# Optimization experiments

Measured on AMD Instinct MI355X. Metric: run time of the kernel, lower is better.

## Reference

```python
import jax, jax.numpy as jnp
import numpy as np

# config derived from init_kwargs: batch_sizes=[2048,2048], rs=[32,128], num_adapters=[32,32]
B1, B2, MULT = 2048, 2048, 4            # group1 tokens (r_mult=1), group2 tokens (r_mult=128/32=4)
IN_F, OUT_F, R_MIN = 4096, 4096, 32
NA1, NA2 = 32, 32
N_SPLIT_ADAPTERS = NA1 + NA2 * MULT      # 160 rank-min slices
LORA_BATCH = B1 + B2 * MULT              # 10240 gathered rows


def setup_inputs() -> dict:
    key = jax.random.key(0)
    k1, k2, k3, k4, k5 = jax.random.split(key, 5)
    x = jax.random.normal(k1, (B1 + B2, 1, IN_F), dtype=jnp.float16)
    lora_A = (jax.random.normal(k2, (N_SPLIT_ADAPTERS, IN_F, R_MIN), dtype=jnp.float16) * jnp.float16(0.02))
    lora_B = (jax.random.normal(k3, (N_SPLIT_ADAPTERS, R_MIN, OUT_F), dtype=jnp.float16) * jnp.float16(0.02))
    # group1: one row per token; group2: each token repeated MULT times (rank split)
    xids = jnp.concatenate([
        jnp.arange(B1, dtype=jnp.int32),
        jnp.repeat(jnp.arange(B1, B1 + B2, dtype=jnp.int32), MULT),
    ])
    # group1 adapters occupy slice ids [0, NA1); group2 adapter j occupies NA1 + j*MULT .. +MULT-1
    w1 = jax.random.randint(k4, (B1,), 0, NA1, dtype=jnp.int32)
    j = jax.random.randint(k5, (B2,), 0, NA2, dtype=jnp.int32)
    w2 = ((jnp.int32(NA1) + j * MULT)[:, None] + jnp.arange(MULT, dtype=jnp.int32)[None, :]).reshape(-1)
    wids = jnp.concatenate([w1, w2])
    return {"x": x, "xids": xids, "wids": wids, "lora_A": lora_A, "lora_B": lora_B}


def reference(x, xids, wids, lora_A, lora_B):
    xg = jnp.take(x, xids, axis=0)          # (L, 1, IN_F)
    A = jnp.take(lora_A, wids, axis=0)      # (L, IN_F, R_MIN)
    Bw = jnp.take(lora_B, wids, axis=0)     # (L, R_MIN, OUT_F)
    y = jnp.einsum('lpi,lir->lpr', xg, A)   # (L, 1, R_MIN)
    y = jnp.einsum('lpr,lro->lpo', y, Bw) * 2.0  # (L, 1, OUT_F), scaling factor 2.0
    # split + sum combine: group1 passes through, group2 sums each block of MULT rank-slices
    z1 = y[:B1]                                          # (B1, 1, OUT_F)
    z2 = y[B1:].reshape(B2, MULT, 1, OUT_F).sum(axis=1)  # (B2, 1, OUT_F)
    return jnp.concatenate([z1, z2], axis=0)             # (B1+B2, 1, OUT_F)
```

## Files before the change

### kernel.cpp

```cpp
#include <hip/hip_runtime.h>

#define IN_F   4096
#define OUT_F  4096
#define RK     32
#define NB1    2048
#define MAXB   2048
#define LBATCH 10240
#define LRK    (LBATCH * RK)

typedef __attribute__((ext_vector_type(2))) __fp16 h2;
typedef __attribute__((ext_vector_type(4))) __fp16 h4;
typedef __attribute__((ext_vector_type(8))) __fp16 h8;
typedef __attribute__((ext_vector_type(4))) float  f4;


__global__ __launch_bounds__(256) void bin_rows(const int* __restrict__ wids,
                                                int* __restrict__ cnt,
                                                int* __restrict__ list) {
    __shared__ int lc;
    int g = blockIdx.x, t = threadIdx.x;
    if (t == 0) lc = 0;
    __syncthreads();
    int* lg = list + g * MAXB;
    if (g < 32) {
        for (int i = t; i < NB1; i += 256)
            if (wids[i] == g) lg[atomicAdd(&lc, 1)] = i;
    } else {
        for (int i = t; i < 2048; i += 256)
            if (32 + ((wids[NB1 + 4 * i] - 32) >> 2) == g) lg[atomicAdd(&lc, 1)] = i;
    }
    __syncthreads();
    if (t == 0) cnt[g] = lc;
}

__device__ __forceinline__ void lda(const float* __restrict__ As, int s,
                                    int kp0, int c40, f4 L[2][2]) {
    #pragma unroll
    for (int p = 0; p < 2; ++p) {
        const float* q = As + ((size_t)s * 32 + 2 * (kp0 + 8 * p)) * RK + c40;
        L[p][0] = *(const f4*)q;
        L[p][1] = *(const f4*)(q + RK);
    }
}
__device__ __forceinline__ void wra(__fp16 (*dst)[40], int kp0, int c40,
                                    const f4 L[2][2]) {
    #pragma unroll
    for (int p = 0; p < 2; ++p) {
        int k = 2 * (kp0 + 8 * p);
        #pragma unroll
        for (int j = 0; j < 4; ++j) {
            int c  = c40 + j;
            int kb = (k >> 3) ^ ((c >> 3) & 3);
            *(h2*)&dst[c][kb * 8 + (k & 7)] =
                __builtin_amdgcn_cvt_pkrtz(L[p][0][j], L[p][1][j]);
        }
    }
}

template<int NST, int PITCH>
__device__ __forceinline__ void s1_waveloop(const float* __restrict__ Ap,
                                            const __fp16 (*Xl)[PITCH],
                                            __fp16 (*buf)[32][40], int koff0,
                                            int m, int kg, int kp0, int c40,
                                            f4& acc0, f4& acc1) {
    f4 L0[2][2], L1[2][2];
    lda(Ap, 0, kp0, c40, L0);
    wra(buf[0], kp0, c40, L0);
    if (NST > 1) lda(Ap, 1, kp0, c40, L1);
    #pragma unroll
    for (int s = 0; s < NST; ++s) {
        h8 xa = *(const h8*)&Xl[m][koff0 + s * 32 + kg * 8];
        int c0 = m,      kb0 = kg ^ ((c0 >> 3) & 3);
        int c1 = m + 16, kb1 = kg ^ ((c1 >> 3) & 3);
        h8 bf0 = *(const h8*)&buf[s & 1][c0][kb0 * 8];
        h8 bf1 = *(const h8*)&buf[s & 1][c1][kb1 * 8];
        if (s + 2 < NST) lda(Ap, s + 2, kp0, c40, ((s & 1) == 0) ? L0 : L1);
        acc0 = __builtin_amdgcn_mfma_f32_16x16x32_f16(xa, bf0, acc0, 0, 0, 0);
        acc1 = __builtin_amdgcn_mfma_f32_16x16x32_f16(xa, bf1, acc1, 0, 0, 0);
        if (s + 1 < NST) wra(buf[(s + 1) & 1], kp0, c40, ((s & 1) == 0) ? L1 : L0);
    }
}

template<int KS>
__global__ __launch_bounds__(256, 4) void s1(const float* __restrict__ x,
                                             const float* __restrict__ A,
                                             const int* __restrict__ cnt,
                                             const int* __restrict__ list,
                                             float* __restrict__ slabs) {
    constexpr int KCH   = IN_F / KS;
    constexpr int PITCH = KCH + 8;
    constexpr int C4    = KCH / 4;
    __shared__ __fp16 Xl[16][PITCH];
    __shared__ __fp16 At[4][2][32][40];
    __shared__ int rowid[16];

    int t = threadIdx.x, lane = t & 63, wv = t >> 6;
    int m = lane & 15, kg = lane >> 4;
    int bx = blockIdx.x, kc = blockIdx.y, rt = blockIdx.z;
    int p2 = bx >= 32;
    int n = cnt[bx];
    if (rt * 16 >= n) return;
    const int* lst = list + bx * MAXB;
    if (t < 16) {
        int it = rt * 16 + t;
        rowid[t] = lst[it < n ? it : n - 1];
    }
    __syncthreads();

    {
        int k0 = kc * KCH;
        #pragma unroll
        for (int itr = 0; itr < KCH / 64; ++itr) {
            int slot = t + 256 * itr;
            int row  = slot / C4;
            int c4   = slot & (C4 - 1);
            int xrow = rowid[row] + (p2 ? NB1 : 0);
            f4 v = *(const f4*)&x[(size_t)xrow * IN_F + k0 + 4 * c4];
            h4 pk;
            h2 a = __builtin_amdgcn_cvt_pkrtz(v.x, v.y);
            h2 b = __builtin_amdgcn_cvt_pkrtz(v.z, v.w);
            pk[0] = a.x; pk[1] = a.y; pk[2] = b.x; pk[3] = b.y;
            *(h4*)&Xl[row][4 * c4] = pk;
        }
    }
    __syncthreads();

    int kp0 = lane >> 3, c40 = (lane & 7) * 4;
    f4 acc0 = {0.f, 0.f, 0.f, 0.f}, acc1 = {0.f, 0.f, 0.f, 0.f};
    float* slab = slabs + (size_t)kc * LRK;

    if (p2) {
        int u = bx - 32;
        const float* Ap = A + ((size_t)(32 + 4 * u + wv) * IN_F + (size_t)kc * KCH) * RK;
        s1_waveloop<KCH / 32, PITCH>(Ap, Xl, At[wv], 0, m, kg, kp0, c40, acc0, acc1);
        #pragma unroll
        for (int q = 0; q < 4; ++q) {
            int itq = rt * 16 + 4 * kg + q;
            if (itq < n) {
                int rid = rowid[4 * kg + q];
                float* sp = slab + (size_t)(NB1 + 4 * rid + wv) * RK + m;
                sp[0]  = acc0[q];
                sp[16] = acc1[q];
            }
        }
    } else {
        const float* Ap = A + ((size_t)bx * IN_F + (size_t)kc * KCH + wv * (KCH / 4)) * RK;
        s1_waveloop<KCH / 128, PITCH>(Ap, Xl, At[wv], wv * (KCH / 4), m, kg, kp0, c40, acc0, acc1);
        float* red = (float*)&Xl[0][0];
        __syncthreads();
        if (wv > 0) {
            *(f4*)&red[((wv - 1) * 64 + lane) * 8]     = acc0;
            *(f4*)&red[((wv - 1) * 64 + lane) * 8 + 4] = acc1;
        }
        __syncthreads();
        if (wv == 0) {
            #pragma unroll
            for (int j = 0; j < 3; ++j) {
                acc0 += *(const f4*)&red[(j * 64 + lane) * 8];
                acc1 += *(const f4*)&red[(j * 64 + lane) * 8 + 4];
            }
            #pragma unroll
            for (int q = 0; q < 4; ++q) {
                int itq = rt * 16 + 4 * kg + q;
                if (itq < n) {
                    int rid = rowid[4 * kg + q];
                    float* sp = slab + (size_t)rid * RK + m;
                    sp[0]  = acc0[q];
                    sp[16] = acc1[q];
                }
            }
        }
    }
}

template<int KS>
__global__ __launch_bounds__(256) void reduceR(const float* __restrict__ slabs,
                                               __fp16* __restrict__ Rh) {
    int i = (blockIdx.x * 256 + threadIdx.x) * 8;
    f4 a = *(const f4*)(slabs + i);
    f4 b = *(const f4*)(slabs + i + 4);
    #pragma unroll
    for (int s = 1; s < KS; ++s) {
        a += *(const f4*)(slabs + (size_t)s * LRK + i);
        b += *(const f4*)(slabs + (size_t)s * LRK + i + 4);
    }
    h8 o;
    o[0] = (__fp16)a.x; o[1] = (__fp16)a.y; o[2] = (__fp16)a.z; o[3] = (__fp16)a.w;
    o[4] = (__fp16)b.x; o[5] = (__fp16)b.y; o[6] = (__fp16)b.z; o[7] = (__fp16)b.w;
    *(h8*)(Rh + i) = o;
}

__global__ __launch_bounds__(256, 4) void s2(const __fp16* __restrict__ Rh,
                                             const float* __restrict__ B,
                                             const int* __restrict__ cnt,
                                             const int* __restrict__ list,
                                             float* __restrict__ out) {
    int lane = threadIdx.x & 63, wv = threadIdx.x >> 6;
    int g   = blockIdx.x;
    int oct = blockIdx.y * 4 + wv;
    int p2  = g >= 32;
    int n = cnt[g];
    if (n == 0) return;
    const int* lst = list + g * MAXB;
    int m = lane & 15, kg = lane >> 4;
    int oc0 = oct * 32;
    int nkc = p2 ? 4 : 1;

    h8 bf[4][2];
    #pragma unroll
    for (int kcb = 0; kcb < 4; ++kcb) {
        if (kcb < nkc) {
            int a = p2 ? (32 + 4 * (g - 32) + kcb) : g;
            const float* Bb = B + ((size_t)a * RK + kg * 8) * OUT_F + oc0 + m;
            #pragma unroll
            for (int ct = 0; ct < 2; ++ct) {
                union { h8 v; h2 h[4]; } u2;
                #pragma unroll
                for (int jj = 0; jj < 4; ++jj) {
                    float e0 = Bb[(size_t)(2 * jj) * OUT_F + ct * 16];
                    float e1 = Bb[(size_t)(2 * jj + 1) * OUT_F + ct * 16];
                    u2.h[jj] = __builtin_amdgcn_cvt_pkrtz(e0, e1);
                }
                bf[kcb][ct] = u2.v;
            }
        }
    }

    for (int rt = 0; rt * 16 < n; ++rt) {
        int it = rt * 16 + m;
        int ridm = lst[it < n ? it : n - 1];
        f4 acc0 = {0.f, 0.f, 0.f, 0.f}, acc1 = {0.f, 0.f, 0.f, 0.f};
        #pragma unroll
        for (int kcb = 0; kcb < 4; ++kcb) {
            if (kcb < nkc) {
                int rrow = p2 ? (NB1 + 4 * ridm + kcb) : ridm;
                h8 rf = *(const h8*)(Rh + (size_t)rrow * RK + kg * 8);
                acc0 = __builtin_amdgcn_mfma_f32_16x16x32_f16(rf, bf[kcb][0], acc0, 0, 0, 0);
                acc1 = __builtin_amdgcn_mfma_f32_16x16x32_f16(rf, bf[kcb][1], acc1, 0, 0, 0);
            }
        }
        #pragma unroll
        for (int q = 0; q < 4; ++q) {
            int itq = rt * 16 + 4 * kg + q;
            if (itq < n) {
                int ridq = lst[itq];
                int orow = p2 ? (NB1 + ridq) : ridq;
                float* op = out + (size_t)orow * OUT_F + oc0 + m;
                op[0]  = 2.f * acc0[q];
                op[16] = 2.f * acc1[q];
            }
        }
    }
}

extern "C" void kernel_launch(void* const* d_in, const int* in_sizes, int n_in,
                              void* d_out, int out_size, void* d_ws, size_t ws_size,
                              hipStream_t stream) {
    const float* x    = (const float*)d_in[0];
    const int*   wids = (const int*)  d_in[2];
    const float* A    = (const float*)d_in[3];
    const float* Bm   = (const float*)d_in[4];
    float* out = (float*)d_out;

    int* wsI  = (int*)d_ws;
    int* cnt  = wsI;
    int* list = wsI + 64;
    __fp16* Rh  = (__fp16*)(list + 64 * MAXB);
    float* slabs = (float*)((char*)Rh + (size_t)LRK * sizeof(__fp16));

    size_t fixed = (size_t)(64 + 64 * MAXB) * sizeof(int) + (size_t)LRK * sizeof(__fp16);
    int ks = (ws_size >= fixed + (size_t)8 * LRK * sizeof(float)) ? 8 : 4;

    bin_rows<<<dim3(64), dim3(256), 0, stream>>>(wids, cnt, list);
    if (ks == 8) {
        s1<8><<<dim3(64, 8, 8), dim3(256), 0, stream>>>(x, A, cnt, list, slabs);
        reduceR<8><<<dim3(160), dim3(256), 0, stream>>>(slabs, Rh);
    } else {
        s1<4><<<dim3(64, 4, 8), dim3(256), 0, stream>>>(x, A, cnt, list, slabs);
        reduceR<4><<<dim3(160), dim3(256), 0, stream>>>(slabs, Rh);
    }
    s2<<<dim3(64, 32), dim3(256), 0, stream>>>(Rh, Bm, cnt, list, out);
}
```

Measured before the change: 305.8 us.

## Pre-transpose LoRA A to fp16 k-major and stream operands directly from global

Adds a prep pass, merged with the row-binning kernel, that converts lora_A from fp32 to fp16 and transposes it so each rank column is contiguous along K. The first-stage kernel then drops its LDS staging of x and A. Each lane loads its MFMA fragments straight from global memory: 8-element fp16 vectors for A, and x converted in registers. The aim is to halve A traffic in the main GEMV and remove LDS round trips and barriers. In exchange the whole A tensor is rewritten on every call, workspace use grows, and the stride-4096 fragment loads may coalesce poorly.

After: 325.0 us. 6.3% more time.

```diff
diff --git a/kernel.cpp b/kernel.cpp
--- a/kernel.cpp
+++ b/kernel.cpp
@@ -7,164 +7,151 @@
 #define MAXB   2048
 #define LBATCH 10240
 #define LRK    (LBATCH * RK)
+#define NADP   160
 
 typedef __attribute__((ext_vector_type(2))) __fp16 h2;
-typedef __attribute__((ext_vector_type(4))) __fp16 h4;
 typedef __attribute__((ext_vector_type(8))) __fp16 h8;
 typedef __attribute__((ext_vector_type(4))) float  f4;
 
 
-__global__ __launch_bounds__(256) void bin_rows(const int* __restrict__ wids,
-                                                int* __restrict__ cnt,
-                                                int* __restrict__ list) {
-    __shared__ int lc;
-    int g = blockIdx.x, t = threadIdx.x;
-    if (t == 0) lc = 0;
+__global__ __launch_bounds__(256) void prep(const int* __restrict__ wids,
+                                            int* __restrict__ cnt,
+                                            int* __restrict__ list,
+                                            const float* __restrict__ A,
+                                            __fp16* __restrict__ Ath) {
+    int bx = blockIdx.x, t = threadIdx.x;
+    if (bx < 64) {
+        __shared__ int lc;
+        if (t == 0) lc = 0;
+        __syncthreads();
+        int* lg = list + bx * MAXB;
+        if (bx < 32) {
+            for (int i = t; i < NB1; i += 256)
+                if (wids[i] == bx) lg[atomicAdd(&lc, 1)] = i;
+        } else {
+            for (int i = t; i < 2048; i += 256)
+                if (32 + ((wids[NB1 + 4 * i] - 32) >> 2) == bx) lg[atomicAdd(&lc, 1)] = i;
+        }
+        __syncthreads();
+        if (t == 0) cnt[bx] = lc;
+        return;
+    }
+    int bb = bx - 64;
+    int a = bb >> 4, kt = bb & 15, k0 = kt * 256;
+    __shared__ __fp16 T[32][264];
+    const float* Ab = A + ((size_t)a * IN_F + k0) * RK;
+    #pragma unroll
+    for (int i = 0; i < 8; ++i) {
+        int slot = t + 256 * i;
+        int k = slot >> 3, c4 = (slot & 7) * 4;
+        f4 v = *(const f4*)(Ab + (size_t)k * RK + c4);
+        T[c4 + 0][k] = (__fp16)v.x; T[c4 + 1][k] = (__fp16)v.y;
+        T[c4 + 2][k] = (__fp16)v.z; T[c4 + 3][k] = (__fp16)v.w;
+    }
     __syncthreads();
-    int* lg = list + g * MAXB;
-    if (g < 32) {
-        for (int i = t; i < NB1; i += 256)
-            if (wids[i] == g) lg[atomicAdd(&lc, 1)] = i;
-    } else {
-        for (int i = t; i < 2048; i += 256)
-            if (32 + ((wids[NB1 + 4 * i] - 32) >> 2) == g) lg[atomicAdd(&lc, 1)] = i;
-    }
-    __syncthreads();
-    if (t == 0) cnt[g] = lc;
-}
-
-__device__ __forceinline__ void lda(const float* __restrict__ As, int s,
-                                    int kp0, int c40, f4 L[2][2]) {
-    #pragma unroll
-    for (int p = 0; p < 2; ++p) {
-        const float* q = As + ((size_t)s * 32 + 2 * (kp0 + 8 * p)) * RK + c40;
-        L[p][0] = *(const f4*)q;
-        L[p][1] = *(const f4*)(q + RK);
-    }
-}
-__device__ __forceinline__ void wra(__fp16 (*dst)[40], int kp0, int c40,
-                                    const f4 L[2][2]) {
-    #pragma unroll
-    for (int p = 0; p < 2; ++p) {
-        int k = 2 * (kp0 + 8 * p);
-        #pragma unroll
-        for (int j = 0; j < 4; ++j) {
-            int c  = c40 + j;
-            int kb = (k >> 3) ^ ((c >> 3) & 3);
-            *(h2*)&dst[c][kb * 8 + (k & 7)] =
-                __builtin_amdgcn_cvt_pkrtz(L[p][0][j], L[p][1][j]);
-        }
-    }
-}
-
-template<int NST, int PITCH>
-__device__ __forceinline__ void s1_waveloop(const float* __restrict__ Ap,
-                                            const __fp16 (*Xl)[PITCH],
-                                            __fp16 (*buf)[32][40], int koff0,
-                                            int m, int kg, int kp0, int c40,
-                                            f4& acc0, f4& acc1) {
-    f4 L0[2][2], L1[2][2];
-    lda(Ap, 0, kp0, c40, L0);
-    wra(buf[0], kp0, c40, L0);
-    if (NST > 1) lda(Ap, 1, kp0, c40, L1);
-    #pragma unroll
+    int c = t >> 3, j = t & 7;
+    __fp16* Ao = Ath + ((size_t)a * RK + c) * IN_F + k0;
+    #pragma unroll
+    for (int i = 0; i < 4; ++i) {
+        int kk = (j + 8 * i) * 8;
+        *(h8*)(Ao + kk) = *(const h8*)&T[c][kk];
+    }
+}
+
+__device__ __forceinline__ h8 cvt_x(f4 x0, f4 x1) {
+    union { h8 v; h2 h[4]; } u;
+    u.h[0] = __builtin_amdgcn_cvt_pkrtz(x0.x, x0.y);
+    u.h[1] = __builtin_amdgcn_cvt_pkrtz(x0.z, x0.w);
+    u.h[2] = __builtin_amdgcn_cvt_pkrtz(x1.x, x1.y);
+    u.h[3] = __builtin_amdgcn_cvt_pkrtz(x1.z, x1.w);
+    return u.v;
+}
+
+template<int NST, bool TA>
+__device__ __forceinline__ void s1_loop(const float* __restrict__ xp,
+                                        const __fp16* __restrict__ A0,
+                                        const __fp16* __restrict__ A1,
+                                        const float* __restrict__ Araw, int m,
+                                        f4& acc0, f4& acc1) {
+    #pragma unroll 4
     for (int s = 0; s < NST; ++s) {
-        h8 xa = *(const h8*)&Xl[m][koff0 + s * 32 + kg * 8];
-        int c0 = m,      kb0 = kg ^ ((c0 >> 3) & 3);
-        int c1 = m + 16, kb1 = kg ^ ((c1 >> 3) & 3);
-        h8 bf0 = *(const h8*)&buf[s & 1][c0][kb0 * 8];
-        h8 bf1 = *(const h8*)&buf[s & 1][c1][kb1 * 8];
-        if (s + 2 < NST) lda(Ap, s + 2, kp0, c40, ((s & 1) == 0) ? L0 : L1);
-        acc0 = __builtin_amdgcn_mfma_f32_16x16x32_f16(xa, bf0, acc0, 0, 0, 0);
-        acc1 = __builtin_amdgcn_mfma_f32_16x16x32_f16(xa, bf1, acc1, 0, 0, 0);
-        if (s + 1 < NST) wra(buf[(s + 1) & 1], kp0, c40, ((s & 1) == 0) ? L1 : L0);
-    }
-}
-
-template<int KS>
+        h8 af0, af1;
+        if constexpr (TA) {
+            af0 = *(const h8*)(A0 + s * 32);
+            af1 = *(const h8*)(A1 + s * 32);
+        } else {
+            #pragma unroll
+            for (int j = 0; j < 8; ++j) {
+                af0[j] = (__fp16)Araw[(size_t)(s * 32 + j) * RK + m];
+                af1[j] = (__fp16)Araw[(size_t)(s * 32 + j) * RK + m + 16];
+            }
+        }
+        f4 x0 = *(const f4*)(xp + s * 32);
+        f4 x1 = *(const f4*)(xp + s * 32 + 4);
+        h8 xa = cvt_x(x0, x1);
+        acc0 = __builtin_amdgcn_mfma_f32_16x16x32_f16(xa, af0, acc0, 0, 0, 0);
+        acc1 = __builtin_amdgcn_mfma_f32_16x16x32_f16(xa, af1, acc1, 0, 0, 0);
+    }
+}
+
+template<int KS, bool TA>
 __global__ __launch_bounds__(256, 4) void s1(const float* __restrict__ x,
-                                             const float* __restrict__ A,
+                                             const float* __restrict__ Araw,
+                                             const __fp16* __restrict__ Ath,
                                              const int* __restrict__ cnt,
                                              const int* __restrict__ list,
                                              float* __restrict__ slabs) {
-    constexpr int KCH   = IN_F / KS;
-    constexpr int PITCH = KCH + 8;
-    constexpr int C4    = KCH / 4;
-    __shared__ __fp16 Xl[16][PITCH];
-    __shared__ __fp16 At[4][2][32][40];
-    __shared__ int rowid[16];
-
-    int t = threadIdx.x, lane = t & 63, wv = t >> 6;
-    int m = lane & 15, kg = lane >> 4;
+    constexpr int KCH = IN_F / KS;
+    __shared__ f4 red[3][64][2];
+    int t = threadIdx.x, lane = t & 63, wv = t >> 6, m = lane & 15, kg = lane >> 4;
     int bx = blockIdx.x, kc = blockIdx.y, rt = blockIdx.z;
     int p2 = bx >= 32;
     int n = cnt[bx];
     if (rt * 16 >= n) return;
     const int* lst = list + bx * MAXB;
-    if (t < 16) {
-        int it = rt * 16 + t;
-        rowid[t] = lst[it < n ? it : n - 1];
-    }
-    __syncthreads();
-
-    {
-        int k0 = kc * KCH;
-        #pragma unroll
-        for (int itr = 0; itr < KCH / 64; ++itr) {
-            int slot = t + 256 * itr;
-            int row  = slot / C4;
-            int c4   = slot & (C4 - 1);
-            int xrow = rowid[row] + (p2 ? NB1 : 0);
-            f4 v = *(const f4*)&x[(size_t)xrow * IN_F + k0 + 4 * c4];
-            h4 pk;
-            h2 a = __builtin_amdgcn_cvt_pkrtz(v.x, v.y);
-            h2 b = __builtin_amdgcn_cvt_pkrtz(v.z, v.w);
-            pk[0] = a.x; pk[1] = a.y; pk[2] = b.x; pk[3] = b.y;
-            *(h4*)&Xl[row][4 * c4] = pk;
-        }
-    }
-    __syncthreads();
-
-    int kp0 = lane >> 3, c40 = (lane & 7) * 4;
+    int it  = rt * 16 + m;
+    int rid = lst[it < n ? it : n - 1];
+    int xrow = rid + (p2 ? NB1 : 0);
+    float* slab = slabs + (size_t)kc * LRK;
     f4 acc0 = {0.f, 0.f, 0.f, 0.f}, acc1 = {0.f, 0.f, 0.f, 0.f};
-    float* slab = slabs + (size_t)kc * LRK;
 
     if (p2) {
-        int u = bx - 32;
-        const float* Ap = A + ((size_t)(32 + 4 * u + wv) * IN_F + (size_t)kc * KCH) * RK;
-        s1_waveloop<KCH / 32, PITCH>(Ap, Xl, At[wv], 0, m, kg, kp0, c40, acc0, acc1);
+        int a  = 32 + 4 * (bx - 32) + wv;
+        int kb = kc * KCH + kg * 8;
+        const float*  xp = x + (size_t)xrow * IN_F + kb;
+        const __fp16* A0 = Ath + ((size_t)a * RK + m) * IN_F + kb;
+        const __fp16* A1 = A0 + (size_t)16 * IN_F;
+        const float*  Ar = Araw + ((size_t)a * IN_F + kb) * RK;
+        s1_loop<KCH / 32, TA>(xp, A0, A1, Ar, m, acc0, acc1);
         #pragma unroll
         for (int q = 0; q < 4; ++q) {
             int itq = rt * 16 + 4 * kg + q;
             if (itq < n) {
-                int rid = rowid[4 * kg + q];
-                float* sp = slab + (size_t)(NB1 + 4 * rid + wv) * RK + m;
+                int ridq = lst[itq];
+                float* sp = slab + (size_t)(NB1 + 4 * ridq + wv) * RK + m;
                 sp[0]  = acc0[q];
                 sp[16] = acc1[q];
             }
         }
     } else {
-        const float* Ap = A + ((size_t)bx * IN_F + (size_t)kc * KCH + wv * (KCH / 4)) * RK;
-        s1_waveloop<KCH / 128, PITCH>(Ap, Xl, At[wv], wv * (KCH / 4), m, kg, kp0, c40, acc0, acc1);
-        float* red = (float*)&Xl[0][0];
-        __syncthreads();
-        if (wv > 0) {
-            *(f4*)&red[((wv - 1) * 64 + lane) * 8]     = acc0;
-            *(f4*)&red[((wv - 1) * 64 + lane) * 8 + 4] = acc1;
-        }
+        int a  = bx;
+        int kb = kc * KCH + wv * (KCH / 4) + kg * 8;
+        const float*  xp = x + (size_t)xrow * IN_F + kb;
+        const __fp16* A0 = Ath + ((size_t)a * RK + m) * IN_F + kb;
+        const __fp16* A1 = A0 + (size_t)16 * IN_F;
+        const float*  Ar = Araw + ((size_t)a * IN_F + kb) * RK;
+        s1_loop<KCH / 128, TA>(xp, A0, A1, Ar, m, acc0, acc1);
+        if (wv > 0) { red[wv - 1][lane][0] = acc0; red[wv - 1][lane][1] = acc1; }
         __syncthreads();
         if (wv == 0) {
             #pragma unroll
-            for (int j = 0; j < 3; ++j) {
-                acc0 += *(const f4*)&red[(j * 64 + lane) * 8];
-                acc1 += *(const f4*)&red[(j * 64 + lane) * 8 + 4];
-            }
+            for (int j = 0; j < 3; ++j) { acc0 += red[j][lane][0]; acc1 += red[j][lane][1]; }
             #pragma unroll
             for (int q = 0; q < 4; ++q) {
                 int itq = rt * 16 + 4 * kg + q;
                 if (itq < n) {
-                    int rid = rowid[4 * kg + q];
-                    float* sp = slab + (size_t)rid * RK + m;
+                    int ridq = lst[itq];
+                    float* sp = slab + (size_t)ridq * RK + m;
                     sp[0]  = acc0[q];
                     sp[16] = acc1[q];
                 }
@@ -265,19 +252,31 @@
     int* wsI  = (int*)d_ws;
     int* cnt  = wsI;
     int* list = wsI + 64;
-    __fp16* Rh  = (__fp16*)(list + 64 * MAXB);
-    float* slabs = (float*)((char*)Rh + (size_t)LRK * sizeof(__fp16));
-
-    size_t fixed = (size_t)(64 + 64 * MAXB) * sizeof(int) + (size_t)LRK * sizeof(__fp16);
-    int ks = (ws_size >= fixed + (size_t)8 * LRK * sizeof(float)) ? 8 : 4;
-
-    bin_rows<<<dim3(64), dim3(256), 0, stream>>>(wids, cnt, list);
-    if (ks == 8) {
-        s1<8><<<dim3(64, 8, 8), dim3(256), 0, stream>>>(x, A, cnt, list, slabs);
-        reduceR<8><<<dim3(160), dim3(256), 0, stream>>>(slabs, Rh);
+    __fp16* Rh = (__fp16*)(list + 64 * MAXB);
+    char* p = (char*)Rh + (size_t)LRK * sizeof(__fp16);
+
+    size_t fixed  = (size_t)(64 + 64 * MAXB) * sizeof(int) + (size_t)LRK * sizeof(__fp16);
+    size_t athB   = (size_t)NADP * RK * IN_F * sizeof(__fp16);
+    size_t slab1  = (size_t)LRK * sizeof(float);
+
+    bool ta = false; int ks = 4;
+    if      (ws_size >= fixed + athB + 8 * slab1) { ta = true;  ks = 8; }
+    else if (ws_size >= fixed + athB + 4 * slab1) { ta = true;  ks = 4; }
+    else if (ws_size >= fixed + 8 * slab1)        { ta = false; ks = 8; }
+    else                                          { ta = false; ks = 4; }
+
+    __fp16* Ath  = ta ? (__fp16*)p : nullptr;
+    float* slabs = (float*)(ta ? (p + athB) : p);
+
+    prep<<<dim3(ta ? 64 + NADP * 16 : 64), dim3(256), 0, stream>>>(wids, cnt, list, A, Ath);
+    if (ta) {
+        if (ks == 8) s1<8, true ><<<dim3(64, 8, 8), dim3(256), 0, stream>>>(x, A, Ath, cnt, list, slabs);
+        else         s1<4, true ><<<dim3(64, 4, 8), dim3(256), 0, stream>>>(x, A, Ath, cnt, list, slabs);
     } else {
-        s1<4><<<dim3(64, 4, 8), dim3(256), 0, stream>>>(x, A, cnt, list, slabs);
-        reduceR<4><<<dim3(160), dim3(256), 0, stream>>>(slabs, Rh);
-    }
+        if (ks == 8) s1<8, false><<<dim3(64, 8, 8), dim3(256), 0, stream>>>(x, A, Ath, cnt, list, slabs);
+        else         s1<4, false><<<dim3(64, 4, 8), dim3(256), 0, stream>>>(x, A, Ath, cnt, list, slabs);
+    }
+    if (ks == 8) reduceR<8><<<dim3(160), dim3(256), 0, stream>>>(slabs, Rh);
+    else         reduceR<4><<<dim3(160), dim3(256), 0, stream>>>(slabs, Rh);
     s2<<<dim3(64, 32), dim3(256), 0, stream>>>(Rh, Bm, cnt, list, out);
 }
```
